# Kernel tuning notes

Hardware: AMD Instinct MI355X
Metric: run time of the kernel (lower is better)

The kernel has to match this reference:

```python
import jax, jax.numpy as jnp
import numpy as np

DELTA_V = 0.5
DELTA_D = 1.5
LOSS_WEIGHT = 1.0


def setup_inputs() -> dict:
    key = jax.random.key(0)
    k1, k2, k3, k4 = jax.random.split(key, 4)
    B, D, H, W = 8, 4, 640, 640
    return {
        "emb": jax.random.normal(k1, (B, D, H, W), dtype=jnp.float32),
        "instance": jax.random.randint(k2, (B, H, W), 0, 33, dtype=jnp.int32),
        "kernel": jax.random.uniform(k3, (B, H, W), dtype=jnp.float32),
        "training_mask": jax.random.uniform(k4, (B, H, W), dtype=jnp.float32),
        "num_labels": 33,  # static: background label 0 + 32 instances, all present w.h.p.
    }


def _single(emb, instance, kernel, tmask, num_labels):
    # emb: [D,H,W]; instance: [H,W] int; kernel/tmask: [H,W] float
    D = emb.shape[0]
    tm = (tmask > 0.5).astype(instance.dtype)
    kn = (kernel > 0.5).astype(instance.dtype)
    inst2 = instance * tm                      # instance masked by training mask
    inst_k = (inst2 * kn).reshape(-1)          # kernel-restricted labels, [N]
    inst = inst2.reshape(-1)                   # [N]
    x = emb.reshape(D, -1).T                   # [N, D]
    ones = jnp.ones(x.shape[0], jnp.float32)

    # per-instance kernel means (scatter-mean), label 0 column forced to zero
    sums = jax.ops.segment_sum(x, inst_k, num_segments=num_labels)      # [K1, D]
    cnts = jax.ops.segment_sum(ones, inst_k, num_segments=num_labels)   # [K1]
    mean = sums / jnp.maximum(cnts, 1.0)[:, None]
    mean = mean.at[0].set(0.0)

    # aggregation term: per-pixel distance to its instance mean, segmented mean over labels 1..K
    diff = x - mean[inst]                                               # [N, D]
    dist = jnp.sqrt(jnp.sum(diff * diff, axis=1))
    val = jnp.log(jnp.maximum(dist - DELTA_V, 0.0) ** 2 + 1.0)
    cnt_i = jax.ops.segment_sum(ones, inst, num_segments=num_labels)
    agg = jax.ops.segment_sum(val, inst, num_segments=num_labels) / jnp.maximum(cnt_i, 1.0)
    l_agg = jnp.mean(agg[1:])

    # discrimination term: pairwise distances between instance means (exclude label 0 and diagonal)
    m = mean[1:]                                                        # [K, D]
    K = m.shape[0]
    pdiff = m[:, None, :] - m[None, :, :]
    pd = jnp.sqrt(jnp.sum(pdiff * pdiff, axis=-1) + jnp.eye(K))         # diag padded (masked below)
    vald = jnp.log(jnp.maximum(2.0 * DELTA_D - pd, 0.0) ** 2 + 1.0)
    off = 1.0 - jnp.eye(K)
    l_dis = jnp.sum(vald * off) / (K * (K - 1))

    # regularizer: mean over all num_labels columns; label-0 column contributes log(1)=0
    nrm1 = jnp.sqrt(jnp.sum(m * m, axis=1))
    l_reg = jnp.sum(jnp.log(nrm1 + 1.0)) / num_labels * 0.001

    return l_agg + l_dis + l_reg


def reference(emb, instance, kernel, training_mask, num_labels):
    f = lambda e, i, k, t: _single(e, i, k, t, num_labels)
    loss_batch = jax.vmap(f)(emb, instance, kernel, training_mask)
    return jnp.mean(LOSS_WEIGHT * loss_batch)
```

## Files before the change

kernel.cpp:

```cpp
#include <hip/hip_runtime.h>
#include <math.h>

#define HW    409600
#define HW4   102400
#define BATCH 8
#define NLAB  33
#define WSF   231

__global__ void init_ws(float* ws) {
    int i = blockIdx.x * 256 + threadIdx.x;
    if (i < BATCH * WSF) ws[i] = 0.f;
}

__device__ __forceinline__ void acc1(int iv, float kv, float tv,
                                     float x0, float x1, float x2, float x3,
                                     float* bins) {
    int lab = (tv > 0.5f) ? iv : 0;
    if (lab != 0) {
        float* bb = bins + lab * 6;
        atomicAdd(bb + 5, 1.f);
        if (kv > 0.5f) {
            atomicAdd(bb + 0, x0);
            atomicAdd(bb + 1, x1);
            atomicAdd(bb + 2, x2);
            atomicAdd(bb + 3, x3);
            atomicAdd(bb + 4, 1.f);
        }
    }
}

__global__ __launch_bounds__(256) void pass1(const float* __restrict__ emb,
                                             const int*   __restrict__ inst,
                                             const float* __restrict__ kern,
                                             const float* __restrict__ tmask,
                                             float*       __restrict__ ws) {
    __shared__ float bins[4][NLAB * 6];
    int t = threadIdx.x, b = blockIdx.y, wave = t >> 6;
    for (int i = t; i < 4 * NLAB * 6; i += 256) (&bins[0][0])[i] = 0.f;
    __syncthreads();

    const float4* emb4  = (const float4*)(emb  + (size_t)b * 4 * HW);
    const int4*   inst4 = (const int4*)  (inst + (size_t)b * HW);
    const float4* kern4 = (const float4*)(kern + (size_t)b * HW);
    const float4* tm4   = (const float4*)(tmask+ (size_t)b * HW);
    float* mb = bins[wave];

    for (int p = blockIdx.x * 256 + t; p < HW4; p += gridDim.x * 256) {
        int4   iv = inst4[p];
        float4 kv = kern4[p];
        float4 tv = tm4[p];
        float4 x0 = emb4[p];
        float4 x1 = emb4[p + HW4];
        float4 x2 = emb4[p + 2 * HW4];
        float4 x3 = emb4[p + 3 * HW4];
        acc1(iv.x, kv.x, tv.x, x0.x, x1.x, x2.x, x3.x, mb);
        acc1(iv.y, kv.y, tv.y, x0.y, x1.y, x2.y, x3.y, mb);
        acc1(iv.z, kv.z, tv.z, x0.z, x1.z, x2.z, x3.z, mb);
        acc1(iv.w, kv.w, tv.w, x0.w, x1.w, x2.w, x3.w, mb);
    }
    __syncthreads();

    float* w = ws + b * WSF;
    for (int i = t; i < NLAB * 6; i += 256) {
        float v = bins[0][i] + bins[1][i] + bins[2][i] + bins[3][i];
        if (v != 0.f) {
            int lab = i / 6, f = i % 6;
            int dst = (f < 4) ? lab * 4 + f : (f == 4 ? 132 + lab : 165 + lab);
            atomicAdd(w + dst, v);
        }
    }
}

__global__ __launch_bounds__(256) void pass2(const float* __restrict__ emb,
                                             const int*   __restrict__ inst,
                                             const float* __restrict__ tmask,
                                             float*       __restrict__ ws) {
    __shared__ float mean_s[NLAB][4];
    __shared__ float vb[4][NLAB];
    int t = threadIdx.x, b = blockIdx.y, wave = t >> 6;
    float* w = ws + b * WSF;

    if (t < NLAB) {
        float inv = 1.f / fmaxf(w[132 + t], 1.f);
        float z = (t == 0) ? 0.f : 1.f;
        mean_s[t][0] = z * w[t * 4 + 0] * inv;
        mean_s[t][1] = z * w[t * 4 + 1] * inv;
        mean_s[t][2] = z * w[t * 4 + 2] * inv;
        mean_s[t][3] = z * w[t * 4 + 3] * inv;
    }
    for (int i = t; i < 4 * NLAB; i += 256) (&vb[0][0])[i] = 0.f;
    __syncthreads();

    const float4* emb4  = (const float4*)(emb  + (size_t)b * 4 * HW);
    const int4*   inst4 = (const int4*)  (inst + (size_t)b * HW);
    const float4* tm4   = (const float4*)(tmask+ (size_t)b * HW);
    float* mv = vb[wave];

    for (int p = blockIdx.x * 256 + t; p < HW4; p += gridDim.x * 256) {
        int4   iv = inst4[p];
        float4 tv = tm4[p];
        float4 x0 = emb4[p];
        float4 x1 = emb4[p + HW4];
        float4 x2 = emb4[p + 2 * HW4];
        float4 x3 = emb4[p + 3 * HW4];
        #pragma unroll
        for (int e = 0; e < 4; ++e) {
            int   ivv = (e == 0) ? iv.x : (e == 1) ? iv.y : (e == 2) ? iv.z : iv.w;
            float tvv = (e == 0) ? tv.x : (e == 1) ? tv.y : (e == 2) ? tv.z : tv.w;
            float a0  = (e == 0) ? x0.x : (e == 1) ? x0.y : (e == 2) ? x0.z : x0.w;
            float a1  = (e == 0) ? x1.x : (e == 1) ? x1.y : (e == 2) ? x1.z : x1.w;
            float a2  = (e == 0) ? x2.x : (e == 1) ? x2.y : (e == 2) ? x2.z : x2.w;
            float a3  = (e == 0) ? x3.x : (e == 1) ? x3.y : (e == 2) ? x3.z : x3.w;
            int lab = (tvv > 0.5f) ? ivv : 0;
            if (lab != 0) {
                float d0 = a0 - mean_s[lab][0];
                float d1 = a1 - mean_s[lab][1];
                float d2 = a2 - mean_s[lab][2];
                float d3 = a3 - mean_s[lab][3];
                float dist = sqrtf(d0 * d0 + d1 * d1 + d2 * d2 + d3 * d3);
                float u = fmaxf(dist - 0.5f, 0.f);
                atomicAdd(mv + lab, logf(u * u + 1.f));
            }
        }
    }
    __syncthreads();
    for (int i = t; i < NLAB; i += 256) {
        float v = vb[0][i] + vb[1][i] + vb[2][i] + vb[3][i];
        if (v != 0.f) atomicAdd(w + 198 + i, v);
    }
}

__global__ __launch_bounds__(256) void final_kernel(const float* __restrict__ ws,
                                                    float* __restrict__ out) {
    __shared__ float mean_s[NLAB][4];
    __shared__ float red[256];
    int t = threadIdx.x;
    float total = 0.f;
    for (int b = 0; b < BATCH; ++b) {
        const float* w = ws + b * WSF;
        if (t < NLAB) {
            float inv = 1.f / fmaxf(w[132 + t], 1.f);
            float z = (t == 0) ? 0.f : 1.f;
            mean_s[t][0] = z * w[t * 4 + 0] * inv;
            mean_s[t][1] = z * w[t * 4 + 1] * inv;
            mean_s[t][2] = z * w[t * 4 + 2] * inv;
            mean_s[t][3] = z * w[t * 4 + 3] * inv;
        }
        __syncthreads();
        float part = 0.f;
        if (t >= 1 && t < NLAB) {
            float ci = fmaxf(w[165 + t], 1.f);
            part = (w[198 + t] / ci) * (1.f / 32.f);
        }
        float disp = 0.f;
        for (int p = t; p < 1024; p += 256) {
            int i = p >> 5, j = p & 31;
            if (i != j) {
                float d0 = mean_s[i + 1][0] - mean_s[j + 1][0];
                float d1 = mean_s[i + 1][1] - mean_s[j + 1][1];
                float d2 = mean_s[i + 1][2] - mean_s[j + 1][2];
                float d3 = mean_s[i + 1][3] - mean_s[j + 1][3];
                float pd = sqrtf(d0 * d0 + d1 * d1 + d2 * d2 + d3 * d3);
                float u = fmaxf(2.0f * 1.5f - pd, 0.f);
                disp += logf(u * u + 1.f);
            }
        }
        disp *= 1.f / (32.f * 31.f);
        float regp = 0.f;
        if (t >= 1 && t < NLAB) {
            float n2 = mean_s[t][0] * mean_s[t][0] + mean_s[t][1] * mean_s[t][1] +
                       mean_s[t][2] * mean_s[t][2] + mean_s[t][3] * mean_s[t][3];
            regp = logf(sqrtf(n2) + 1.f) * (0.001f / 33.f);
        }
        red[t] = part + disp + regp;
        __syncthreads();
        for (int s = 128; s > 0; s >>= 1) {
            if (t < s) red[t] += red[t + s];
            __syncthreads();
        }
        if (t == 0) total += red[0];
        __syncthreads();
    }
    if (t == 0) out[0] = total * (1.f / BATCH);
}

extern "C" void kernel_launch(void* const* d_in, const int* in_sizes, int n_in,
                              void* d_out, int out_size, void* d_ws, size_t ws_size,
                              hipStream_t stream) {
    const float* emb   = (const float*)d_in[0];
    const int*   inst  = (const int*)  d_in[1];
    const float* kern  = (const float*)d_in[2];
    const float* tmask = (const float*)d_in[3];
    float* ws  = (float*)d_ws;
    float* out = (float*)d_out;

    init_ws<<<dim3((BATCH * WSF + 255) / 256), 256, 0, stream>>>(ws);
    dim3 grid(128, BATCH);
    pass1<<<grid, 256, 0, stream>>>(emb, inst, kern, tmask, ws);
    pass2<<<grid, 256, 0, stream>>>(emb, inst, tmask, ws);
    final_kernel<<<1, 256, 0, stream>>>(ws, out);
}
```

Measured before the change: 173.7 us.

## Fuse both passes and final reduction into one persistent kernel with grid barriers

Merges pass1, pass2 and the final kernel into a single launch. Blocks synchronise through global atomic barriers, and each block keeps its tile of packed labels in LDS so pass2 does not reread instance and mask data. Pass1 loads embeddings only for groups that contain kernel pixels, and pass2 only for labelled pixels. Shared-memory bins are replicated 8 ways to cut atomic contention, and the per-label aggregation is pre-scaled so a single scalar is accumulated. The grid barrier requires all 1024 blocks to be co-resident, or the kernel deadlocks, and fast __logf changes precision slightly.

```diff
diff --git a/kernel.cpp b/kernel.cpp
--- a/kernel.cpp
+++ b/kernel.cpp
@@ -1,176 +1,221 @@
 #include <hip/hip_runtime.h>
 #include <math.h>
 
-#define HW    409600
-#define HW4   102400
-#define BATCH 8
-#define NLAB  33
-#define WSF   231
+#define HW      409600
+#define HW4     102400
+#define BATCH   8
+#define NLAB    33
+#define GX      128
+#define NBLOCK  (GX*BATCH)
+#define GPB     (HW4/GX)
+#define NREP    8
+#define RS      201
+#define WSB     208
+#define BAR_OFF (WSB*BATCH)
 
 __global__ void init_ws(float* ws) {
     int i = blockIdx.x * 256 + threadIdx.x;
-    if (i < BATCH * WSF) ws[i] = 0.f;
-}
-
-__device__ __forceinline__ void acc1(int iv, float kv, float tv,
-                                     float x0, float x1, float x2, float x3,
-                                     float* bins) {
-    int lab = (tv > 0.5f) ? iv : 0;
-    if (lab != 0) {
-        float* bb = bins + lab * 6;
-        atomicAdd(bb + 5, 1.f);
-        if (kv > 0.5f) {
-            atomicAdd(bb + 0, x0);
-            atomicAdd(bb + 1, x1);
-            atomicAdd(bb + 2, x2);
-            atomicAdd(bb + 3, x3);
-            atomicAdd(bb + 4, 1.f);
-        }
-    }
-}
-
-__global__ __launch_bounds__(256) void pass1(const float* __restrict__ emb,
-                                             const int*   __restrict__ inst,
-                                             const float* __restrict__ kern,
-                                             const float* __restrict__ tmask,
-                                             float*       __restrict__ ws) {
-    __shared__ float bins[4][NLAB * 6];
-    int t = threadIdx.x, b = blockIdx.y, wave = t >> 6;
-    for (int i = t; i < 4 * NLAB * 6; i += 256) (&bins[0][0])[i] = 0.f;
-    __syncthreads();
-
-    const float4* emb4  = (const float4*)(emb  + (size_t)b * 4 * HW);
-    const int4*   inst4 = (const int4*)  (inst + (size_t)b * HW);
-    const float4* kern4 = (const float4*)(kern + (size_t)b * HW);
-    const float4* tm4   = (const float4*)(tmask+ (size_t)b * HW);
-    float* mb = bins[wave];
-
-    for (int p = blockIdx.x * 256 + t; p < HW4; p += gridDim.x * 256) {
-        int4   iv = inst4[p];
-        float4 kv = kern4[p];
-        float4 tv = tm4[p];
-        float4 x0 = emb4[p];
-        float4 x1 = emb4[p + HW4];
-        float4 x2 = emb4[p + 2 * HW4];
-        float4 x3 = emb4[p + 3 * HW4];
-        acc1(iv.x, kv.x, tv.x, x0.x, x1.x, x2.x, x3.x, mb);
-        acc1(iv.y, kv.y, tv.y, x0.y, x1.y, x2.y, x3.y, mb);
-        acc1(iv.z, kv.z, tv.z, x0.z, x1.z, x2.z, x3.z, mb);
-        acc1(iv.w, kv.w, tv.w, x0.w, x1.w, x2.w, x3.w, mb);
-    }
-    __syncthreads();
-
-    float* w = ws + b * WSF;
+    if (i < BAR_OFF + 8) ws[i] = 0.f;
+}
+
+__device__ __forceinline__ void bar_arrive(unsigned* cnt) {
+    __syncthreads();
+    if (threadIdx.x == 0)
+        __hip_atomic_fetch_add(cnt, 1u, __ATOMIC_RELEASE, __HIP_MEMORY_SCOPE_AGENT);
+}
+__device__ __forceinline__ void bar_wait(unsigned* cnt, unsigned n) {
+    if (threadIdx.x == 0) {
+        while (__hip_atomic_load(cnt, __ATOMIC_ACQUIRE, __HIP_MEMORY_SCOPE_AGENT) < n)
+            __builtin_amdgcn_s_sleep(4);
+    }
+    __syncthreads();
+}
+
+__device__ __forceinline__ float wsload(const float* p) {
+    return __hip_atomic_load(p, __ATOMIC_RELAXED, __HIP_MEMORY_SCOPE_AGENT);
+}
+
+__global__ __launch_bounds__(256, 4) void fused(const float* __restrict__ emb,
+                                                const int*   __restrict__ inst,
+                                                const float* __restrict__ kern,
+                                                const float* __restrict__ tmask,
+                                                float* ws, float* out) {
+    __shared__ float    bins[NREP][RS];
+    __shared__ unsigned labs[GPB];
+    __shared__ float4   means4[NLAB];
+    __shared__ float    invci[NLAB];
+    __shared__ float    red[256];
+
+    const int t   = threadIdx.x;
+    const int bx  = blockIdx.x;
+    const int b   = blockIdx.y;
+    const int rep = (t >> 3) & (NREP - 1);
+    unsigned* bar = (unsigned*)(ws + BAR_OFF);
+
+    for (int i = t; i < NREP * RS; i += 256) (&bins[0][0])[i] = 0.f;
+    __syncthreads();
+
+    const size_t  base  = (size_t)b * HW;
+    const float4* emb4  = (const float4*)(emb + base * 4);
+    const int4*   inst4 = (const int4*)(inst + base);
+    const float4* kern4 = (const float4*)(kern + base);
+    const float4* tm4   = (const float4*)(tmask + base);
+    const int     g0    = bx * GPB;
+    float*        mb    = bins[rep];
+
+    for (int lg = t; lg < GPB; lg += 256) {
+        const int g = g0 + lg;
+        int4   iv = inst4[g];
+        float4 kv = kern4[g];
+        float4 tv = tm4[g];
+        int l0 = (tv.x > 0.5f) ? iv.x : 0;
+        int l1 = (tv.y > 0.5f) ? iv.y : 0;
+        int l2 = (tv.z > 0.5f) ? iv.z : 0;
+        int l3 = (tv.w > 0.5f) ? iv.w : 0;
+        labs[lg] = (unsigned)l0 | ((unsigned)l1 << 8) |
+                   ((unsigned)l2 << 16) | ((unsigned)l3 << 24);
+        if (l0) atomicAdd(&mb[l0 * 6 + 5], 1.f);
+        if (l1) atomicAdd(&mb[l1 * 6 + 5], 1.f);
+        if (l2) atomicAdd(&mb[l2 * 6 + 5], 1.f);
+        if (l3) atomicAdd(&mb[l3 * 6 + 5], 1.f);
+        bool k0 = l0 && (kv.x > 0.5f);
+        bool k1 = l1 && (kv.y > 0.5f);
+        bool k2 = l2 && (kv.z > 0.5f);
+        bool k3 = l3 && (kv.w > 0.5f);
+        if (k0 | k1 | k2 | k3) {
+            float4 x0 = emb4[g];
+            float4 x1 = emb4[g + HW4];
+            float4 x2 = emb4[g + 2 * HW4];
+            float4 x3 = emb4[g + 3 * HW4];
+            if (k0) {
+                float* bb = &mb[l0 * 6];
+                atomicAdd(bb + 0, x0.x); atomicAdd(bb + 1, x1.x);
+                atomicAdd(bb + 2, x2.x); atomicAdd(bb + 3, x3.x);
+                atomicAdd(bb + 4, 1.f);
+            }
+            if (k1) {
+                float* bb = &mb[l1 * 6];
+                atomicAdd(bb + 0, x0.y); atomicAdd(bb + 1, x1.y);
+                atomicAdd(bb + 2, x2.y); atomicAdd(bb + 3, x3.y);
+                atomicAdd(bb + 4, 1.f);
+            }
+            if (k2) {
+                float* bb = &mb[l2 * 6];
+                atomicAdd(bb + 0, x0.z); atomicAdd(bb + 1, x1.z);
+                atomicAdd(bb + 2, x2.z); atomicAdd(bb + 3, x3.z);
+                atomicAdd(bb + 4, 1.f);
+            }
+            if (k3) {
+                float* bb = &mb[l3 * 6];
+                atomicAdd(bb + 0, x0.w); atomicAdd(bb + 1, x1.w);
+                atomicAdd(bb + 2, x2.w); atomicAdd(bb + 3, x3.w);
+                atomicAdd(bb + 4, 1.f);
+            }
+        }
+    }
+    __syncthreads();
+
+    float* w = ws + b * WSB;
     for (int i = t; i < NLAB * 6; i += 256) {
-        float v = bins[0][i] + bins[1][i] + bins[2][i] + bins[3][i];
+        float v = 0.f;
+        #pragma unroll
+        for (int r = 0; r < NREP; ++r) v += bins[r][i];
         if (v != 0.f) {
             int lab = i / 6, f = i % 6;
-            int dst = (f < 4) ? lab * 4 + f : (f == 4 ? 132 + lab : 165 + lab);
+            int dst = (f < 4) ? lab * 4 + f : ((f == 4) ? 132 + lab : 165 + lab);
             atomicAdd(w + dst, v);
         }
     }
-}
-
-__global__ __launch_bounds__(256) void pass2(const float* __restrict__ emb,
-                                             const int*   __restrict__ inst,
-                                             const float* __restrict__ tmask,
-                                             float*       __restrict__ ws) {
-    __shared__ float mean_s[NLAB][4];
-    __shared__ float vb[4][NLAB];
-    int t = threadIdx.x, b = blockIdx.y, wave = t >> 6;
-    float* w = ws + b * WSF;
+
+    bar_arrive(&bar[0]);
+    bar_wait(&bar[0], NBLOCK);
 
     if (t < NLAB) {
-        float inv = 1.f / fmaxf(w[132 + t], 1.f);
+        float inv = 1.f / fmaxf(wsload(w + 132 + t), 1.f);
         float z = (t == 0) ? 0.f : 1.f;
-        mean_s[t][0] = z * w[t * 4 + 0] * inv;
-        mean_s[t][1] = z * w[t * 4 + 1] * inv;
-        mean_s[t][2] = z * w[t * 4 + 2] * inv;
-        mean_s[t][3] = z * w[t * 4 + 3] * inv;
-    }
-    for (int i = t; i < 4 * NLAB; i += 256) (&vb[0][0])[i] = 0.f;
-    __syncthreads();
-
-    const float4* emb4  = (const float4*)(emb  + (size_t)b * 4 * HW);
-    const int4*   inst4 = (const int4*)  (inst + (size_t)b * HW);
-    const float4* tm4   = (const float4*)(tmask+ (size_t)b * HW);
-    float* mv = vb[wave];
-
-    for (int p = blockIdx.x * 256 + t; p < HW4; p += gridDim.x * 256) {
-        int4   iv = inst4[p];
-        float4 tv = tm4[p];
-        float4 x0 = emb4[p];
-        float4 x1 = emb4[p + HW4];
-        float4 x2 = emb4[p + 2 * HW4];
-        float4 x3 = emb4[p + 3 * HW4];
-        #pragma unroll
-        for (int e = 0; e < 4; ++e) {
-            int   ivv = (e == 0) ? iv.x : (e == 1) ? iv.y : (e == 2) ? iv.z : iv.w;
-            float tvv = (e == 0) ? tv.x : (e == 1) ? tv.y : (e == 2) ? tv.z : tv.w;
-            float a0  = (e == 0) ? x0.x : (e == 1) ? x0.y : (e == 2) ? x0.z : x0.w;
-            float a1  = (e == 0) ? x1.x : (e == 1) ? x1.y : (e == 2) ? x1.z : x1.w;
-            float a2  = (e == 0) ? x2.x : (e == 1) ? x2.y : (e == 2) ? x2.z : x2.w;
-            float a3  = (e == 0) ? x3.x : (e == 1) ? x3.y : (e == 2) ? x3.z : x3.w;
-            int lab = (tvv > 0.5f) ? ivv : 0;
-            if (lab != 0) {
-                float d0 = a0 - mean_s[lab][0];
-                float d1 = a1 - mean_s[lab][1];
-                float d2 = a2 - mean_s[lab][2];
-                float d3 = a3 - mean_s[lab][3];
-                float dist = sqrtf(d0 * d0 + d1 * d1 + d2 * d2 + d3 * d3);
-                float u = fmaxf(dist - 0.5f, 0.f);
-                atomicAdd(mv + lab, logf(u * u + 1.f));
-            }
-        }
-    }
-    __syncthreads();
-    for (int i = t; i < NLAB; i += 256) {
-        float v = vb[0][i] + vb[1][i] + vb[2][i] + vb[3][i];
-        if (v != 0.f) atomicAdd(w + 198 + i, v);
-    }
-}
-
-__global__ __launch_bounds__(256) void final_kernel(const float* __restrict__ ws,
-                                                    float* __restrict__ out) {
-    __shared__ float mean_s[NLAB][4];
-    __shared__ float red[256];
-    int t = threadIdx.x;
+        float4 m;
+        m.x = z * wsload(w + t * 4 + 0) * inv;
+        m.y = z * wsload(w + t * 4 + 1) * inv;
+        m.z = z * wsload(w + t * 4 + 2) * inv;
+        m.w = z * wsload(w + t * 4 + 3) * inv;
+        means4[t] = m;
+        invci[t]  = 1.f / fmaxf(wsload(w + 165 + t), 1.f);
+    }
+    __syncthreads();
+
+    float acc = 0.f;
+    for (int lg = t; lg < GPB; lg += 256) {
+        unsigned pk = labs[lg];
+        if (pk) {
+            const int g = g0 + lg;
+            float4 x0 = emb4[g];
+            float4 x1 = emb4[g + HW4];
+            float4 x2 = emb4[g + 2 * HW4];
+            float4 x3 = emb4[g + 3 * HW4];
+            #pragma unroll
+            for (int e = 0; e < 4; ++e) {
+                int l = (pk >> (8 * e)) & 255;
+                if (l) {
+                    float a0 = (e == 0) ? x0.x : (e == 1) ? x0.y : (e == 2) ? x0.z : x0.w;
+                    float a1 = (e == 0) ? x1.x : (e == 1) ? x1.y : (e == 2) ? x1.z : x1.w;
+                    float a2 = (e == 0) ? x2.x : (e == 1) ? x2.y : (e == 2) ? x2.z : x2.w;
+                    float a3 = (e == 0) ? x3.x : (e == 1) ? x3.y : (e == 2) ? x3.z : x3.w;
+                    float4 m = means4[l];
+                    float d0 = a0 - m.x, d1 = a1 - m.y, d2 = a2 - m.z, d3 = a3 - m.w;
+                    float dist = sqrtf(d0 * d0 + d1 * d1 + d2 * d2 + d3 * d3);
+                    float u = fmaxf(dist - 0.5f, 0.f);
+                    acc += __logf(u * u + 1.f) * invci[l];
+                }
+            }
+        }
+    }
+    red[t] = acc;
+    __syncthreads();
+    for (int s = 128; s > 0; s >>= 1) {
+        if (t < s) red[t] += red[t + s];
+        __syncthreads();
+    }
+    if (t == 0) atomicAdd(w + 198, red[0]);
+
+    bar_arrive(&bar[1]);
+    if (bx != 0 || b != 0) return;
+    bar_wait(&bar[1], NBLOCK);
+
     float total = 0.f;
-    for (int b = 0; b < BATCH; ++b) {
-        const float* w = ws + b * WSF;
+    for (int bb = 0; bb < BATCH; ++bb) {
+        const float* wb = ws + bb * WSB;
+        __syncthreads();
         if (t < NLAB) {
-            float inv = 1.f / fmaxf(w[132 + t], 1.f);
+            float inv = 1.f / fmaxf(wsload(wb + 132 + t), 1.f);
             float z = (t == 0) ? 0.f : 1.f;
-            mean_s[t][0] = z * w[t * 4 + 0] * inv;
-            mean_s[t][1] = z * w[t * 4 + 1] * inv;
-            mean_s[t][2] = z * w[t * 4 + 2] * inv;
-            mean_s[t][3] = z * w[t * 4 + 3] * inv;
+            float4 m;
+            m.x = z * wsload(wb + t * 4 + 0) * inv;
+            m.y = z * wsload(wb + t * 4 + 1) * inv;
+            m.z = z * wsload(wb + t * 4 + 2) * inv;
+            m.w = z * wsload(wb + t * 4 + 3) * inv;
+            means4[t] = m;
         }
         __syncthreads();
         float part = 0.f;
-        if (t >= 1 && t < NLAB) {
-            float ci = fmaxf(w[165 + t], 1.f);
-            part = (w[198 + t] / ci) * (1.f / 32.f);
-        }
+        if (t == 0) part = wsload(wb + 198) * (1.f / 32.f);
         float disp = 0.f;
         for (int p = t; p < 1024; p += 256) {
             int i = p >> 5, j = p & 31;
             if (i != j) {
-                float d0 = mean_s[i + 1][0] - mean_s[j + 1][0];
-                float d1 = mean_s[i + 1][1] - mean_s[j + 1][1];
-                float d2 = mean_s[i + 1][2] - mean_s[j + 1][2];
-                float d3 = mean_s[i + 1][3] - mean_s[j + 1][3];
+                float4 mi = means4[i + 1], mj = means4[j + 1];
+                float d0 = mi.x - mj.x, d1 = mi.y - mj.y;
+                float d2 = mi.z - mj.z, d3 = mi.w - mj.w;
                 float pd = sqrtf(d0 * d0 + d1 * d1 + d2 * d2 + d3 * d3);
-                float u = fmaxf(2.0f * 1.5f - pd, 0.f);
-                disp += logf(u * u + 1.f);
-            }
-        }
-        disp *= 1.f / (32.f * 31.f);
+                float u = fmaxf(3.0f - pd, 0.f);
+                disp += __logf(u * u + 1.f);
+            }
+        }
+        disp *= 1.f / 992.f;
         float regp = 0.f;
         if (t >= 1 && t < NLAB) {
-            float n2 = mean_s[t][0] * mean_s[t][0] + mean_s[t][1] * mean_s[t][1] +
-                       mean_s[t][2] * mean_s[t][2] + mean_s[t][3] * mean_s[t][3];
-            regp = logf(sqrtf(n2) + 1.f) * (0.001f / 33.f);
+            float4 m = means4[t];
+            float n2 = m.x * m.x + m.y * m.y + m.z * m.z + m.w * m.w;
+            regp = __logf(sqrtf(n2) + 1.f) * (0.001f / 33.f);
         }
         red[t] = part + disp + regp;
         __syncthreads();
@@ -179,7 +224,6 @@
             __syncthreads();
         }
         if (t == 0) total += red[0];
-        __syncthreads();
     }
     if (t == 0) out[0] = total * (1.f / BATCH);
 }
@@ -194,9 +238,6 @@
     float* ws  = (float*)d_ws;
     float* out = (float*)d_out;
 
-    init_ws<<<dim3((BATCH * WSF + 255) / 256), 256, 0, stream>>>(ws);
-    dim3 grid(128, BATCH);
-    pass1<<<grid, 256, 0, stream>>>(emb, inst, kern, tmask, ws);
-    pass2<<<grid, 256, 0, stream>>>(emb, inst, tmask, ws);
-    final_kernel<<<1, 256, 0, stream>>>(ws, out);
-}
+    init_ws<<<dim3((BAR_OFF + 8 + 255) / 256), 256, 0, stream>>>(ws);
+    fused<<<dim3(GX, BATCH), 256, 0, stream>>>(emb, inst, kern, tmask, ws, out);
+}
```

Result: slower. 299.5 us (+72.5%).
